# Kernel optimization log

Measured on AMD Instinct MI355X. Metric: run time of the kernel, lower is better.

Reference implementation:

```python
import jax, jax.numpy as jnp
import numpy as np

B, T, C, H = 16, 4096, 256, 256

def setup_inputs() -> dict:
    key = jax.random.key(0)
    kx, kwi, kbi, kwh, kbh = jax.random.split(key, 5)
    s = 1.0 / np.sqrt(C)
    return {
        "x": jax.random.normal(kx, (B, T, C), dtype=jnp.float32),
        "Wi": jax.random.uniform(kwi, (H, C), dtype=jnp.float32, minval=-s, maxval=s),
        "bi": jax.random.uniform(kbi, (H,), dtype=jnp.float32, minval=-s, maxval=s),
        "Wh": jax.random.uniform(kwh, (H, H), dtype=jnp.float32, minval=-s, maxval=s),
        "bh": jax.random.uniform(kbh, (H,), dtype=jnp.float32, minval=-s, maxval=s),
    }

def reference(x, Wi, bi, Wh, bh):
    # Faithful to the source: Cell computes tanh(i2h(x) + h2h(x)) -- both
    # linears applied to x_t, the hidden state is never consumed, so there
    # is no recurrence and all timesteps can be computed in one fused pass.
    # hidden_states: [B, T, H]
    hidden_states = jnp.tanh(
        jnp.einsum("btc,hc->bth", x, Wi) + bi
        + jnp.einsum("btc,hc->bth", x, Wh) + bh
    )
    h_last = hidden_states[:, -1, :]  # h after the loop
    return (hidden_states, h_last)
```

## Files before the change

kernel.cpp:

```cpp
#include <hip/hip_runtime.h>


using short8 = __attribute__((ext_vector_type(8))) short;
using f32x4  = __attribute__((ext_vector_type(4))) float;

constexpr int Tn = 4096, Cn = 256, Hn = 256;
constexpr int Mn = 16 * Tn;

__device__ inline unsigned pack2_bf16(float a, float b) {
  unsigned ua = __float_as_uint(a);
  unsigned ub = __float_as_uint(b);
  ua += 0x7fffu + ((ua >> 16) & 1u);
  ub += 0x7fffu + ((ub >> 16) & 1u);
  return (ua >> 16) | (ub & 0xffff0000u);
}

union u4s8 { uint4 u; short8 s; };

__global__ __launch_bounds__(256) void prep_kernel(
    const float* __restrict__ Wi, const float* __restrict__ bi,
    const float* __restrict__ Wh, const float* __restrict__ bh,
    unsigned short* __restrict__ Wc, float* __restrict__ bc) {
  int idx = blockIdx.x * 256 + threadIdx.x;
  float w = Wi[idx] + Wh[idx];
  unsigned u = __float_as_uint(w);
  u += 0x7fffu + ((u >> 16) & 1u);
  Wc[idx] = (unsigned short)(u >> 16);
  if (blockIdx.x == 0) bc[threadIdx.x] = bi[threadIdx.x] + bh[threadIdx.x];
}

__global__ __launch_bounds__(256, 2) void gemm_tanh_kernel(
    const float* __restrict__ x, const unsigned short* __restrict__ Wc,
    const float* __restrict__ bc, float* __restrict__ out) {
  __shared__ __align__(16) unsigned short Bsm[128 * 256];

  const int tid   = threadIdx.x;
  const int bid   = blockIdx.x;
  const int mb    = bid & 511;
  const int nb    = bid >> 9;
  const int mBase = mb * 128;
  const int nBase = nb * 128;

  const int wave = tid >> 6;
  const int lane = tid & 63;
  const int rid  = lane & 15;
  const int kgrp = lane >> 4;
  const int rowBase = mBase + wave * 32;

  const float* a0p = x + (size_t)(rowBase + rid) * Cn + kgrp * 8;
  const float* a1p = a0p + (size_t)16 * Cn;
  float4 abuf[8][4];
#pragma unroll
  for (int kc = 0; kc < 8; kc++) {
    const float4* p0 = (const float4*)(a0p + kc * 32);
    const float4* p1 = (const float4*)(a1p + kc * 32);
    abuf[kc][0] = p0[0];
    abuf[kc][1] = p0[1];
    abuf[kc][2] = p1[0];
    abuf[kc][3] = p1[1];
  }

#pragma unroll
  for (int i = 0; i < 16; i++) {
    int h = i * 256 + tid;
    int r = h >> 5;
    int c = h & 31;
    uint4 v = *(const uint4*)(Wc + (size_t)(nBase + r) * Cn + c * 8);
    int pc = c ^ (r & 7);
    *(uint4*)&Bsm[(r << 8) + (pc << 3)] = v;
  }
  __syncthreads();

  f32x4 acc[2][8];
#pragma unroll
  for (int im = 0; im < 2; im++)
#pragma unroll
    for (int in = 0; in < 8; in++) acc[im][in] = (f32x4)0.f;

#pragma unroll
  for (int kc = 0; kc < 8; kc++) {
    u4s8 t0, t1;
    t0.u.x = pack2_bf16(abuf[kc][0].x, abuf[kc][0].y);
    t0.u.y = pack2_bf16(abuf[kc][0].z, abuf[kc][0].w);
    t0.u.z = pack2_bf16(abuf[kc][1].x, abuf[kc][1].y);
    t0.u.w = pack2_bf16(abuf[kc][1].z, abuf[kc][1].w);
    t1.u.x = pack2_bf16(abuf[kc][2].x, abuf[kc][2].y);
    t1.u.y = pack2_bf16(abuf[kc][2].z, abuf[kc][2].w);
    t1.u.z = pack2_bf16(abuf[kc][3].x, abuf[kc][3].y);
    t1.u.w = pack2_bf16(abuf[kc][3].z, abuf[kc][3].w);
    short8 af[2] = {t0.s, t1.s};

    short8 bf[8];
    const int cbase = (kc << 2) | kgrp;
#pragma unroll
    for (int in = 0; in < 8; in++) {
      int ln = in * 16 + rid;
      bf[in] = *(const short8*)&Bsm[(ln << 8) + ((cbase ^ (ln & 7)) << 3)];
    }
#pragma unroll
    for (int im = 0; im < 2; im++)
#pragma unroll
      for (int in = 0; in < 8; in++)
        acc[im][in] = __builtin_amdgcn_mfma_f32_16x16x32_bf16(
            af[im], bf[in], acc[im][in], 0, 0, 0);
  }

#pragma unroll
  for (int in = 0; in < 8; in++) {
    int n = nBase + in * 16 + rid;
    float bias = bc[n];
#pragma unroll
    for (int im = 0; im < 2; im++) {
      int mrow = rowBase + im * 16 + kgrp * 4;
#pragma unroll
      for (int r = 0; r < 4; r++) {
        int m = mrow + r;
        float v = acc[im][in][r] + bias;
        float t = 1.f - 2.f / (__expf(2.f * v) + 1.f);
        __builtin_nontemporal_store(t, &out[(size_t)m * Hn + n]);
        if ((m & (Tn - 1)) == (Tn - 1))
          out[(size_t)Mn * Hn + (size_t)(m >> 12) * Hn + n] = t;
      }
    }
  }
}

extern "C" void kernel_launch(void* const* d_in, const int* in_sizes, int n_in,
                              void* d_out, int out_size, void* d_ws,
                              size_t ws_size, hipStream_t stream) {
  (void)in_sizes; (void)n_in; (void)out_size; (void)ws_size;
  const float* x  = (const float*)d_in[0];
  const float* Wi = (const float*)d_in[1];
  const float* bi = (const float*)d_in[2];
  const float* Wh = (const float*)d_in[3];
  const float* bh = (const float*)d_in[4];
  float* out = (float*)d_out;

  unsigned short* Wc = (unsigned short*)d_ws;
  float* bc = (float*)((char*)d_ws + (size_t)Hn * Cn * sizeof(unsigned short));

  prep_kernel<<<(Hn * Cn) / 256, 256, 0, stream>>>(Wi, bi, Wh, bh, Wc, bc);
  gemm_tanh_kernel<<<1024, 256, 0, stream>>>(x, Wc, bc, out);
}
```

Baseline: 135.9 us.

## Split GEMM tile across eight waves with 16 rows each

Doubles the block to 512 threads so each wave owns 16 output rows instead of 32 of the same 128x128 tile. This halves per-thread A-fragment buffers and accumulators, aiming for more resident waves and more memory-level parallelism. It also replaces the nontemporal output stores with ordinary stores. The launch bound of 4 blocks of 512 threads caps registers per thread, so the 64-float prefetch buffer plus accumulators may spill. The 64KB LDS per block also limits how many blocks can be resident at once.

```diff
diff --git a/kernel.cpp b/kernel.cpp
--- a/kernel.cpp
+++ b/kernel.cpp
@@ -29,7 +29,7 @@
   if (blockIdx.x == 0) bc[threadIdx.x] = bi[threadIdx.x] + bh[threadIdx.x];
 }
 
-__global__ __launch_bounds__(256, 2) void gemm_tanh_kernel(
+__global__ __launch_bounds__(512, 4) void gemm_tanh_kernel(
     const float* __restrict__ x, const unsigned short* __restrict__ Wc,
     const float* __restrict__ bc, float* __restrict__ out) {
   __shared__ __align__(16) unsigned short Bsm[128 * 256];
@@ -45,24 +45,20 @@
   const int lane = tid & 63;
   const int rid  = lane & 15;
   const int kgrp = lane >> 4;
-  const int rowBase = mBase + wave * 32;
+  const int rowBase = mBase + wave * 16;
 
-  const float* a0p = x + (size_t)(rowBase + rid) * Cn + kgrp * 8;
-  const float* a1p = a0p + (size_t)16 * Cn;
-  float4 abuf[8][4];
+  const float* ap = x + (size_t)(rowBase + rid) * Cn + kgrp * 8;
+  float4 abuf[8][2];
 #pragma unroll
   for (int kc = 0; kc < 8; kc++) {
-    const float4* p0 = (const float4*)(a0p + kc * 32);
-    const float4* p1 = (const float4*)(a1p + kc * 32);
-    abuf[kc][0] = p0[0];
-    abuf[kc][1] = p0[1];
-    abuf[kc][2] = p1[0];
-    abuf[kc][3] = p1[1];
+    const float4* p = (const float4*)(ap + kc * 32);
+    abuf[kc][0] = p[0];
+    abuf[kc][1] = p[1];
   }
 
 #pragma unroll
-  for (int i = 0; i < 16; i++) {
-    int h = i * 256 + tid;
+  for (int i = 0; i < 8; i++) {
+    int h = i * 512 + tid;
     int r = h >> 5;
     int c = h & 31;
     uint4 v = *(const uint4*)(Wc + (size_t)(nBase + r) * Cn + c * 8);
@@ -71,56 +67,41 @@
   }
   __syncthreads();
 
-  f32x4 acc[2][8];
+  f32x4 acc[8];
 #pragma unroll
-  for (int im = 0; im < 2; im++)
-#pragma unroll
-    for (int in = 0; in < 8; in++) acc[im][in] = (f32x4)0.f;
+  for (int in = 0; in < 8; in++) acc[in] = (f32x4)0.f;
 
 #pragma unroll
   for (int kc = 0; kc < 8; kc++) {
-    u4s8 t0, t1;
+    u4s8 t0;
     t0.u.x = pack2_bf16(abuf[kc][0].x, abuf[kc][0].y);
     t0.u.y = pack2_bf16(abuf[kc][0].z, abuf[kc][0].w);
     t0.u.z = pack2_bf16(abuf[kc][1].x, abuf[kc][1].y);
     t0.u.w = pack2_bf16(abuf[kc][1].z, abuf[kc][1].w);
-    t1.u.x = pack2_bf16(abuf[kc][2].x, abuf[kc][2].y);
-    t1.u.y = pack2_bf16(abuf[kc][2].z, abuf[kc][2].w);
-    t1.u.z = pack2_bf16(abuf[kc][3].x, abuf[kc][3].y);
-    t1.u.w = pack2_bf16(abuf[kc][3].z, abuf[kc][3].w);
-    short8 af[2] = {t0.s, t1.s};
+    short8 af = t0.s;
 
-    short8 bf[8];
     const int cbase = (kc << 2) | kgrp;
 #pragma unroll
     for (int in = 0; in < 8; in++) {
       int ln = in * 16 + rid;
-      bf[in] = *(const short8*)&Bsm[(ln << 8) + ((cbase ^ (ln & 7)) << 3)];
+      short8 bf = *(const short8*)&Bsm[(ln << 8) + ((cbase ^ (ln & 7)) << 3)];
+      acc[in] = __builtin_amdgcn_mfma_f32_16x16x32_bf16(af, bf, acc[in], 0, 0, 0);
     }
-#pragma unroll
-    for (int im = 0; im < 2; im++)
-#pragma unroll
-      for (int in = 0; in < 8; in++)
-        acc[im][in] = __builtin_amdgcn_mfma_f32_16x16x32_bf16(
-            af[im], bf[in], acc[im][in], 0, 0, 0);
   }
 
 #pragma unroll
   for (int in = 0; in < 8; in++) {
     int n = nBase + in * 16 + rid;
     float bias = bc[n];
+    int mrow = rowBase + kgrp * 4;
 #pragma unroll
-    for (int im = 0; im < 2; im++) {
-      int mrow = rowBase + im * 16 + kgrp * 4;
-#pragma unroll
-      for (int r = 0; r < 4; r++) {
-        int m = mrow + r;
-        float v = acc[im][in][r] + bias;
-        float t = 1.f - 2.f / (__expf(2.f * v) + 1.f);
-        __builtin_nontemporal_store(t, &out[(size_t)m * Hn + n]);
-        if ((m & (Tn - 1)) == (Tn - 1))
-          out[(size_t)Mn * Hn + (size_t)(m >> 12) * Hn + n] = t;
-      }
+    for (int r = 0; r < 4; r++) {
+      int m = mrow + r;
+      float v = acc[in][r] + bias;
+      float t = 1.f - 2.f / (__expf(2.f * v) + 1.f);
+      out[(size_t)m * Hn + n] = t;
+      if ((m & (Tn - 1)) == (Tn - 1))
+        out[(size_t)Mn * Hn + (size_t)(m >> 12) * Hn + n] = t;
     }
   }
 }
@@ -140,5 +121,5 @@
   float* bc = (float*)((char*)d_ws + (size_t)Hn * Cn * sizeof(unsigned short));
 
   prep_kernel<<<(Hn * Cn) / 256, 256, 0, stream>>>(Wi, bi, Wh, bh, Wc, bc);
-  gemm_tanh_kernel<<<1024, 256, 0, stream>>>(x, Wc, bc, out);
+  gemm_tanh_kernel<<<1024, 512, 0, stream>>>(x, Wc, bc, out);
 }
```

Result: no change. 135.3 us (-0.4%).
